# Performance work log

Hardware: AMD Instinct MI355X
Metric: run time of the kernel (lower is better)

Reference implementation:

```python
import jax, jax.numpy as jnp
import numpy as np

B, C, N = 16, 256, 2048
EPS = 1e-5


def setup_inputs() -> dict:
    key = jax.random.key(0)
    ks = jax.random.split(key, 8)
    s = 0.02
    return {
        "x": jax.random.normal(ks[0], (B, C, N), dtype=jnp.float32),
        "w_qkv": jax.random.normal(ks[1], (3 * C, C), dtype=jnp.float32) * s,
        "w_out": jax.random.normal(ks[2], (C, C), dtype=jnp.float32) * s,
        "b_out": jnp.zeros((C,), dtype=jnp.float32),
        "w_conv": jax.random.normal(ks[3], (C, C), dtype=jnp.float32) * s,
        "b_conv": jnp.zeros((C,), dtype=jnp.float32),
        "gamma": jnp.ones((C,), dtype=jnp.float32),
        "beta": jnp.zeros((C,), dtype=jnp.float32),
    }


def reference(x, w_qkv, w_out, b_out, w_conv, b_conv, gamma, beta):
    # x: [B, C, N]
    xt = jnp.swapaxes(x, 1, 2)                      # [B, N, C]
    qkv = jnp.einsum('bnc,dc->bnd', xt, w_qkv)      # [B, N, 3C]
    q, k, v = jnp.split(qkv, 3, axis=-1)
    scale = q.shape[-1] ** -0.5                     # single head, head_dim = C
    scores = jnp.einsum('bic,bjc->bij', q, k) * scale
    attn = jax.nn.softmax(scores, axis=-1)
    x_r = jnp.einsum('bij,bjc->bic', attn, v)
    x_r = jnp.einsum('bnc,oc->bno', x_r, w_out) + b_out  # output projection
    # offset attention: (x_t - x_r), back to [B, C, N]
    d = jnp.swapaxes(xt - x_r, 1, 2)
    # 1x1 conv
    y = jnp.einsum('oc,bcn->bon', w_conv, d) + b_conv[:, None]
    # BatchNorm1d (training-mode batch stats, biased variance)
    mean = jnp.mean(y, axis=(0, 2), keepdims=True)
    var = jnp.var(y, axis=(0, 2), keepdims=True)
    y = (y - mean) * jax.lax.rsqrt(var + EPS)
    y = y * gamma[:, None] + beta[:, None]
    return x + jax.nn.relu(y)
```

## Files before the change

kernel.cpp:

```cpp
#include <hip/hip_runtime.h>

#define BB 16
#define CC 256
#define NN 2048
#define QPRE 0.25f
#define KPRE 0.36067376f

typedef __attribute__((ext_vector_type(8))) short short8;
typedef __attribute__((ext_vector_type(8))) __bf16 bf16x8;
typedef __attribute__((ext_vector_type(4))) short s16x4;
typedef __attribute__((ext_vector_type(4))) float f32x4;
typedef __attribute__((ext_vector_type(16))) float f32x16;
typedef __attribute__((ext_vector_type(4))) int int4v;
typedef __attribute__((ext_vector_type(8))) int int8v;
typedef __attribute__((ext_vector_type(2))) long l64x2;

#define DEVI static __device__ __forceinline__

struct ABArg {
  short8 v;
  __device__ operator short8() const { return v; }
  __device__ operator bf16x8() const { return __builtin_bit_cast(bf16x8, v); }
};

DEVI f32x16 mfma32(short8 a, short8 b, f32x16 c) {
  return __builtin_amdgcn_mfma_f32_32x32x16_bf16(ABArg{a}, ABArg{b}, c, 0, 0, 0);
}
DEVI f32x16 mfma8(long a, long b, f32x16 c) {
  return __builtin_amdgcn_mfma_f32_32x32x16_fp8_fp8(a, b, c, 0, 0, 0);
}
DEVI f32x16 mfma8s(int8v a, int8v b, f32x16 c) {
  return __builtin_amdgcn_mfma_scale_f32_32x32x64_f8f6f4(a, b, c, 0, 0, 0, 127, 0, 127);
}

DEVI unsigned short f2bf(float f) {
  unsigned u = __builtin_bit_cast(unsigned, f);
  u = (u + 0x7fffu + ((u >> 16) & 1u)) >> 16;
  return (unsigned short)u;
}
DEVI float bf2f(unsigned short u) {
  unsigned x = (unsigned)u << 16;
  return __builtin_bit_cast(float, x);
}
DEVI unsigned char f2fp8(float f) {
  int r = __builtin_amdgcn_cvt_pk_fp8_f32(f, f, 0, false);
  return (unsigned char)(r & 0xff);
}
DEVI int psi(int c) { return (c & ~24) | ((c & 8) << 1) | ((c & 16) >> 1); }

DEVI void gl_lds16(const void* g, void* l) {
  __builtin_amdgcn_global_load_lds(
      (const __attribute__((address_space(1))) void*)g,
      (__attribute__((address_space(3))) void*)l, 16, 0, 0);
}

DEVI void stage64(const char* src, char* dst, int tid) {
#pragma unroll
  for (int i = 0; i < 8; i++) {
    int ch = tid + 256 * i;
    int row = ch >> 5, slot = ch & 31;
    gl_lds16(src + (size_t)row * 512 + ((slot * 16) ^ ((row & 7) << 4)), dst + ch * 16);
  }
}

DEVI short8 ldsfrag(const char* lds, int row, int kc, int h) {
  return *(const short8*)(lds + row * 512 + ((kc * 32 + h * 16) ^ ((row & 7) << 4)));
}

DEVI int drow(int r, int h) { return (r & 3) + 8 * (r >> 2) + 4 * h; }

DEVI int8v cat8(int4v lo, int4v hi) {
  int8v v;
  v[0] = lo[0]; v[1] = lo[1]; v[2] = lo[2]; v[3] = lo[3];
  v[4] = hi[0]; v[5] = hi[1]; v[6] = hi[2]; v[7] = hi[3];
  return v;
}

__global__ __launch_bounds__(256) void k_prep(const float* wq, const float* wc, const float* wo,
                                              const float* b_out, const float* b_conv,
                                              unsigned short* wq_b, unsigned short* wc_b,
                                              unsigned short* woT_b, float* biasv) {
  __shared__ float tile[64][65];
  int bx = blockIdx.x;
  if (bx < 768) {
    int i = bx * 256 + threadIdx.x;
    wq_b[i] = f2bf(wq[i]);
    if (i < CC * CC) wc_b[i] = f2bf(wc[i]);
  } else if (bx < 784) {
    int rb = bx - 768;
    int n0 = (rb & 3) * 64, c0 = (rb >> 2) * 64;
    int tcol = threadIdx.x & 63, trq = threadIdx.x >> 6;
#pragma unroll
    for (int rr = 0; rr < 16; rr++) {
      int cl = rr * 4 + trq;
      tile[cl][tcol] = wo[(size_t)(c0 + cl) * CC + n0 + tcol];
    }
    __syncthreads();
#pragma unroll
    for (int rr = 0; rr < 16; rr++) {
      int nl = rr * 4 + trq;
      woT_b[(size_t)(n0 + nl) * CC + c0 + tcol] = f2bf(tile[tcol][nl]);
    }
  } else {
    int o = (bx - 784) * 4 + (threadIdx.x >> 6);
    int lane = threadIdx.x & 63;
    f32x4 wv = *(const f32x4*)(wc + (size_t)o * CC + lane * 4);
    f32x4 bv = *(const f32x4*)(b_out + lane * 4);
    float s = wv[0] * bv[0] + wv[1] * bv[1] + wv[2] * bv[2] + wv[3] * bv[3];
#pragma unroll
    for (int d = 1; d < 64; d <<= 1) s += __shfl_xor(s, d, 64);
    if (lane == 0) biasv[o] = b_conv[o] - s;
  }
}

__global__ __launch_bounds__(256) void k_wcc(const unsigned short* wc_b,
                                             const unsigned short* woT_b, unsigned short* wccN) {
  __shared__ unsigned short WT[64 * 256];
  int o0 = blockIdx.x * 128, c0 = blockIdx.y * 64;
  int tid = threadIdx.x, lane = tid & 63, w = tid >> 6;
  int l31 = lane & 31, h = lane >> 5;
  stage64((const char*)(woT_b + (size_t)c0 * CC), (char*)WT, tid);
  int orow = o0 + w * 32 + l31;
  short8 aw[16];
  const unsigned short* Wp = wc_b + (size_t)orow * CC;
#pragma unroll
  for (int kc = 0; kc < 16; kc++) aw[kc] = *(const short8*)(Wp + kc * 16 + h * 8);
  __syncthreads();
  const char* Wl = (const char*)WT;
  f32x16 acc[2];
#pragma unroll
  for (int t = 0; t < 2; t++) {
#pragma unroll
    for (int r = 0; r < 16; r++) acc[t][r] = 0.f;
#pragma unroll
    for (int kc = 0; kc < 16; kc++)
      acc[t] = mfma32(aw[kc], ldsfrag(Wl, t * 32 + l31, kc, h), acc[t]);
  }
#pragma unroll
  for (int t = 0; t < 2; t++)
#pragma unroll
    for (int r = 0; r < 16; r++) {
      int od = o0 + w * 32 + drow(r, h);
      wccN[(size_t)od * CC + c0 + t * 32 + l31] = f2bf(-acc[t][r]);
    }
}

__global__ __launch_bounds__(256) void k_transpose(const float* x, unsigned short* xt) {
  __shared__ unsigned short tile[64][65];
  int b = blockIdx.z, c0 = blockIdx.y * 64, n0 = blockIdx.x * 64;
  int tcol = threadIdx.x & 63, trq = threadIdx.x >> 6;
  const float* xp = x + (size_t)b * CC * NN;
#pragma unroll
  for (int rr = 0; rr < 16; rr++) {
    int cl = rr * 4 + trq;
    tile[cl][tcol] = f2bf(xp[(size_t)(c0 + cl) * NN + n0 + tcol]);
  }
  __syncthreads();
  unsigned short* xtp = xt + (size_t)b * NN * CC;
#pragma unroll
  for (int rr = 0; rr < 16; rr++) {
    int nl = rr * 4 + trq;
    xtp[(size_t)(n0 + nl) * CC + c0 + tcol] = tile[tcol][nl];
  }
}

__global__ __launch_bounds__(256, 2) void k_qkv(const unsigned short* xt,
                                                const unsigned short* wqkv_b, unsigned char* Qf,
                                                unsigned char* Kf, unsigned char* Vf) {
  __shared__ unsigned short XT[2][64 * 256];
  int o0 = blockIdx.x * 128;
  int tok_base = blockIdx.y * 256;
  int tid = threadIdx.x, lane = tid & 63, w = tid >> 6;
  int l31 = lane & 31, h = lane >> 5;

  short8 aw[16];
  const unsigned short* Wp = wqkv_b + (size_t)(o0 + w * 32 + l31) * CC;
#pragma unroll
  for (int kc = 0; kc < 16; kc++) aw[kc] = *(const short8*)(Wp + kc * 16 + h * 8);

  const char* Xg = (const char*)xt;
  stage64(Xg + (size_t)tok_base * 512, (char*)XT[0], tid);
  __syncthreads();

  int od_l = o0 + w * 32 + l31;
  int psiod = psi(od_l & 255);
  int psil31 = psi(l31);

  int cur = 0;
  for (int tt = 0; tt < 4; tt++) {
    if (tt < 3)
      stage64(Xg + (size_t)(tok_base + (tt + 1) * 64) * 512, (char*)XT[cur ^ 1], tid);
    const char* Xl = (const char*)XT[cur];
    f32x16 acc[2];
#pragma unroll
    for (int t = 0; t < 2; t++)
#pragma unroll
      for (int r = 0; r < 16; r++) acc[t][r] = 0.f;
    if (o0 < 512) {
#pragma unroll
      for (int kc = 0; kc < 16; kc++) {
        acc[0] = mfma32(ldsfrag(Xl, l31, kc, h), aw[kc], acc[0]);
        acc[1] = mfma32(ldsfrag(Xl, 32 + l31, kc, h), aw[kc], acc[1]);
      }
    } else {
#pragma unroll
      for (int kc = 0; kc < 16; kc++) {
        acc[0] = mfma32(aw[kc], ldsfrag(Xl, l31, kc, h), acc[0]);
        acc[1] = mfma32(aw[kc], ldsfrag(Xl, 32 + l31, kc, h), acc[1]);
      }
    }
    int tok0 = tok_base + tt * 64;
    if (o0 < 256) {
#pragma unroll
      for (int t = 0; t < 2; t++)
#pragma unroll
        for (int r = 0; r < 16; r++) {
          int token = tok0 + t * 32 + drow(r, h);
          Qf[(size_t)token * 256 + psiod] = f2fp8(acc[t][r] * QPRE);
        }
    } else if (o0 < 512) {
#pragma unroll
      for (int t = 0; t < 2; t++)
#pragma unroll
        for (int r = 0; r < 16; r++) {
          int token = tok0 + t * 32 + drow(r, h);
          Kf[(size_t)token * 256 + psiod] = f2fp8(acc[t][r]);
        }
    } else {
      int bb = tok0 >> 11;
      int nnb = tok0 & 2047;
#pragma unroll
      for (int t = 0; t < 2; t++)
#pragma unroll
        for (int r = 0; r < 16; r++) {
          int od = o0 + w * 32 + drow(r, h) - 512;
          Vf[(size_t)bb * 256 * NN + (size_t)od * NN + nnb + t * 32 + psil31] = f2fp8(acc[t][r]);
        }
    }
    __syncthreads();
    cur ^= 1;
  }
}

__global__ __launch_bounds__(256, 2) void k_attn(const unsigned char* Qf, const unsigned char* Kf,
                                                 const unsigned char* Vf, unsigned short* AO) {
  __shared__ char SMEM[81920];
  int bid = blockIdx.x;
  int b = bid & 15;
  int q0 = (bid >> 4) * 64;
  int tid = threadIdx.x;
  int lane = tid & 63, w = tid >> 6;
  int g = w >> 1, p = w & 1;
  int gtid = tid & 127;
  int l31 = lane & 31, h = lane >> 5;

  char* G = SMEM + g * 40960;

  int qrow = q0 + p * 32 + l31;
  const unsigned char* Qp = Qf + (size_t)b * NN * 256 + (size_t)qrow * 256;
  int8v q32[4];
#pragma unroll
  for (int m = 0; m < 4; m++) {
    int4v lo = *(const int4v*)(Qp + m * 64 + h * 32);
    int4v hi = *(const int4v*)(Qp + m * 64 + h * 32 + 16);
    q32[m] = cat8(lo, hi);
  }

  f32x16 o[8];
#pragma unroll
  for (int i = 0; i < 8; i++)
#pragma unroll
    for (int r = 0; r < 16; r++) o[i][r] = 0.f;
  float lsum = 0.f;

  const unsigned char* Kg8 = Kf + (size_t)b * NN * 256;
  const unsigned char* Vg8 = Vf + (size_t)b * 256 * NN;
  int jbase = g * 1024;
  int swzk = (l31 & 7) << 4;

  auto stage_k = [&](char* dst, int j0) {
#pragma unroll
    for (int i = 0; i < 4; i++) {
      int ch = gtid + 128 * i;
      int row = ch >> 4, slot = ch & 15;
      gl_lds16(Kg8 + (size_t)(j0 + row) * 256 + ((slot * 16) ^ ((row & 7) << 4)), dst + ch * 16);
    }
  };
  auto stage_v = [&](char* dst, int j0) {
#pragma unroll
    for (int i = 0; i < 4; i++) {
      int ch = gtid + 128 * i;
      int row = ch >> 1, slot = ch & 1;
      gl_lds16(Vg8 + (size_t)row * 2048 + j0 + ((slot * 16) ^ (((row >> 2) & 1) << 4)),
               dst + ch * 16);
    }
  };

  stage_k(G, jbase);
  stage_v(G + 16384, jbase);
  __syncthreads();

  long pf0p = 0, pf1p = 0;
  for (int t = 0; t < 32; t++) {
    char* Kc = G + (t & 1) * 8192;
    if (t < 31) {
      int j0n = jbase + (t + 1) * 32;
      stage_k(G + ((t + 1) & 1) * 8192, j0n);
      stage_v(G + 16384 + ((t + 1) % 3) * 8192, j0n);
    }

    f32x16 s;
#pragma unroll
    for (int r = 0; r < 16; r++) s[r] = 0.f;
    __builtin_amdgcn_s_setprio(1);
#pragma unroll
    for (int m = 0; m < 4; m++) {
      int base = l31 * 256;
      int4v lo = *(const int4v*)(Kc + base + ((m * 64 + h * 32) ^ swzk));
      int4v hi = *(const int4v*)(Kc + base + ((m * 64 + h * 32 + 16) ^ swzk));
      s = mfma8s(cat8(lo, hi), q32[m], s);
    }
    __builtin_amdgcn_s_setprio(0);

    if (t > 0) {
      char* Vp = G + 16384 + ((t - 1) % 3) * 8192;
      int swzv = ((l31 >> 2) & 1) << 4;
      __builtin_amdgcn_s_setprio(1);
#pragma unroll
      for (int ct = 0; ct < 8; ct++) {
        l64x2 vv = *(const l64x2*)(Vp + (ct * 32 + l31) * 32 + ((h * 16) ^ swzv));
        o[ct] = mfma8(pf0p, vv[0], o[ct]);
        o[ct] = mfma8(pf1p, vv[1], o[ct]);
      }
      __builtin_amdgcn_s_setprio(0);
    }

    float pv[16];
    float rsum = 0.f;
#pragma unroll
    for (int r = 0; r < 16; r++) {
      pv[r] = __builtin_amdgcn_exp2f(s[r]);
      rsum += pv[r];
    }
    lsum += rsum;

    int P0 = __builtin_amdgcn_cvt_pk_fp8_f32(pv[0], pv[1], 0, false);
    P0 = __builtin_amdgcn_cvt_pk_fp8_f32(pv[2], pv[3], P0, true);
    int P1 = __builtin_amdgcn_cvt_pk_fp8_f32(pv[4], pv[5], 0, false);
    P1 = __builtin_amdgcn_cvt_pk_fp8_f32(pv[6], pv[7], P1, true);
    int P2 = __builtin_amdgcn_cvt_pk_fp8_f32(pv[8], pv[9], 0, false);
    P2 = __builtin_amdgcn_cvt_pk_fp8_f32(pv[10], pv[11], P2, true);
    int P3 = __builtin_amdgcn_cvt_pk_fp8_f32(pv[12], pv[13], 0, false);
    P3 = __builtin_amdgcn_cvt_pk_fp8_f32(pv[14], pv[15], P3, true);
    int x0 = P0, y0 = P1;
    asm volatile("v_permlane32_swap_b32 %0, %1" : "+v"(x0), "+v"(y0));
    int x1 = P2, y1 = P3;
    asm volatile("v_permlane32_swap_b32 %0, %1" : "+v"(x1), "+v"(y1));
    long pf0c = ((long)(unsigned)y0 << 32) | (unsigned)x0;
    long pf1c = ((long)(unsigned)y1 << 32) | (unsigned)x1;

    __syncthreads();
    pf0p = pf0c;
    pf1p = pf1c;
  }

  {
    char* Vp = G + 16384 + (31 % 3) * 8192;
    int swzv = ((l31 >> 2) & 1) << 4;
#pragma unroll
    for (int ct = 0; ct < 8; ct++) {
      l64x2 vv = *(const l64x2*)(Vp + (ct * 32 + l31) * 32 + ((h * 16) ^ swzv));
      o[ct] = mfma8(pf0p, vv[0], o[ct]);
      o[ct] = mfma8(pf1p, vv[1], o[ct]);
    }
  }

  lsum += __shfl_xor(lsum, 32, 64);
  float* Lx = (float*)SMEM;
  if (h == 0) Lx[w * 32 + l31] = lsum;
  __syncthreads();
  float ltot = lsum + Lx[(w ^ 2) * 32 + l31];
  float linv[16];
#pragma unroll
  for (int r = 0; r < 16; r++) linv[r] = 1.f / __shfl(ltot, drow(r, h), 64);
  __syncthreads();

  char* Rb = SMEM + p * 32768;
  if (g == 1) {
#pragma unroll
    for (int ct = 0; ct < 8; ct++)
#pragma unroll
      for (int k = 0; k < 4; k++) {
        f32x4 v = {o[ct][4 * k], o[ct][4 * k + 1], o[ct][4 * k + 2], o[ct][4 * k + 3]};
        *(f32x4*)(Rb + ((ct * 4 + k) * 64 + lane) * 16) = v;
      }
  }
  __syncthreads();
  if (g == 0) {
    unsigned short* AOp = AO + (size_t)b * NN * CC;
#pragma unroll
    for (int ct = 0; ct < 8; ct++)
#pragma unroll
      for (int k = 0; k < 4; k++) {
        f32x4 qv = *(const f32x4*)(Rb + ((ct * 4 + k) * 64 + lane) * 16);
#pragma unroll
        for (int j = 0; j < 4; j++) {
          int r = 4 * k + j;
          float v = (o[ct][r] + qv[j]) * linv[r];
          AOp[(size_t)(q0 + p * 32 + drow(r, h)) * CC + ct * 32 + l31] = f2bf(v);
        }
      }
  }
}

__global__ __launch_bounds__(256, 1) void k_fused(const unsigned short* xt,
                                                  const unsigned short* AO,
                                                  const unsigned short* wc_b,
                                                  const unsigned short* wccN, const float* biasv,
                                                  unsigned short* yT, float* psum, float* psq) {
  __shared__ unsigned short XT[2][64 * 256], AL[2][64 * 256];
  int o0 = blockIdx.x * 128;
  int tok_base = blockIdx.y * 256;
  int tid = threadIdx.x, lane = tid & 63, w = tid >> 6;
  int l31 = lane & 31, h = lane >> 5;
  int od = o0 + w * 32 + l31;

  short8 aw[32];
  const unsigned short* Wp1 = wc_b + (size_t)od * CC;
  const unsigned short* Wp2 = wccN + (size_t)od * CC;
#pragma unroll
  for (int kc = 0; kc < 16; kc++) {
    aw[kc] = *(const short8*)(Wp1 + kc * 16 + h * 8);
    aw[16 + kc] = *(const short8*)(Wp2 + kc * 16 + h * 8);
  }
  float bias_l = biasv[od];
  float sacc = 0.f, qacc = 0.f;

  const char* Xg = (const char*)xt;
  const char* Ag = (const char*)AO;
  stage64(Xg + (size_t)tok_base * 512, (char*)XT[0], tid);
  stage64(Ag + (size_t)tok_base * 512, (char*)AL[0], tid);
  __syncthreads();

  int cur = 0;
  for (int tt = 0; tt < 4; tt++) {
    if (tt < 3) {
      stage64(Xg + (size_t)(tok_base + (tt + 1) * 64) * 512, (char*)XT[cur ^ 1], tid);
      stage64(Ag + (size_t)(tok_base + (tt + 1) * 64) * 512, (char*)AL[cur ^ 1], tid);
    }
    const char* Xl = (const char*)XT[cur];
    const char* Al = (const char*)AL[cur];
    f32x16 acc[2];
#pragma unroll
    for (int t = 0; t < 2; t++)
#pragma unroll
      for (int r = 0; r < 16; r++) acc[t][r] = 0.f;
#pragma unroll
    for (int kc = 0; kc < 16; kc++) {
      acc[0] = mfma32(ldsfrag(Xl, l31, kc, h), aw[kc], acc[0]);
      acc[1] = mfma32(ldsfrag(Xl, 32 + l31, kc, h), aw[kc], acc[1]);
    }
#pragma unroll
    for (int kc = 0; kc < 16; kc++) {
      acc[0] = mfma32(ldsfrag(Al, l31, kc, h), aw[16 + kc], acc[0]);
      acc[1] = mfma32(ldsfrag(Al, 32 + l31, kc, h), aw[16 + kc], acc[1]);
    }
    int tok0 = tok_base + tt * 64;
#pragma unroll
    for (int t = 0; t < 2; t++)
#pragma unroll
      for (int r = 0; r < 16; r++) {
        float v = acc[t][r] + bias_l;
        sacc += v;
        qacc += v * v;
        int token = tok0 + t * 32 + drow(r, h);
        yT[(size_t)token * CC + od] = f2bf(v);
      }
    __syncthreads();
    cur ^= 1;
  }

  sacc += __shfl_xor(sacc, 32, 64);
  qacc += __shfl_xor(qacc, 32, 64);
  if (h == 0) {
    psum[blockIdx.y * 256 + od] = sacc;
    psq[blockIdx.y * 256 + od] = qacc;
  }
}

__global__ __launch_bounds__(1024) void k_stats2(const float* psum, const float* psq,
                                                 const float* gamma, const float* beta,
                                                 float* scale, float* shift) {
  __shared__ float S4[4][256], Q4[4][256];
  int o = threadIdx.x & 255, part = threadIdx.x >> 8;
  float S = 0.f, Q = 0.f;
  for (int b = part * 32; b < part * 32 + 32; b++) {
    S += psum[b * 256 + o];
    Q += psq[b * 256 + o];
  }
  S4[part][o] = S;
  Q4[part][o] = Q;
  __syncthreads();
  if (part == 0) {
    S = S4[0][o] + S4[1][o] + S4[2][o] + S4[3][o];
    Q = Q4[0][o] + Q4[1][o] + Q4[2][o] + Q4[3][o];
    const float inv = 1.f / (BB * NN);
    float mean = S * inv;
    float var = Q * inv - mean * mean;
    float rstd = rsqrtf(var + 1e-5f);
    float sc = gamma[o] * rstd;
    scale[o] = sc;
    shift[o] = beta[o] - mean * sc;
  }
}

__global__ __launch_bounds__(256) void k_final(const unsigned short* yT, const float* x,
                                               const float* scale, const float* shift, float* out) {
  __shared__ float tile[64][65];
  int n0 = blockIdx.x * 64, c0 = blockIdx.y * 64, b = blockIdx.z;
  int tid = threadIdx.x;
#pragma unroll
  for (int it = 0; it < 2; it++) {
    int rowl = (tid >> 3) + it * 32, slot = tid & 7;
    short8 v = *(const short8*)(yT + (size_t)(b * NN + n0 + rowl) * CC + c0 + slot * 8);
#pragma unroll
    for (int j = 0; j < 8; j++) tile[rowl][slot * 8 + j] = bf2f((unsigned short)v[j]);
  }
  __syncthreads();
  int nl = tid & 63, cg = tid >> 6;
  size_t xb = (size_t)b * CC * NN;
#pragma unroll
  for (int i = 0; i < 16; i++) {
    int cl = cg * 16 + i;
    int c = c0 + cl;
    float v = tile[nl][cl] * scale[c] + shift[c];
    size_t idx = xb + (size_t)c * NN + n0 + nl;
    out[idx] = x[idx] + fmaxf(v, 0.f);
  }
}

extern "C" void kernel_launch(void* const* d_in, const int* in_sizes, int n_in,
                              void* d_out, int out_size, void* d_ws, size_t ws_size,
                              hipStream_t stream) {
  const float* x      = (const float*)d_in[0];
  const float* w_qkv  = (const float*)d_in[1];
  const float* w_out  = (const float*)d_in[2];
  const float* b_out  = (const float*)d_in[3];
  const float* w_conv = (const float*)d_in[4];
  const float* b_conv = (const float*)d_in[5];
  const float* gamma  = (const float*)d_in[6];
  const float* beta   = (const float*)d_in[7];
  float* out = (float*)d_out;

  char* ws = (char*)d_ws;
  size_t off = 0;
  auto take = [&](size_t bytes) -> char* {
    char* p = ws + off;
    off += (bytes + 255) & ~(size_t)255;
    return p;
  };
  const size_t BNC  = (size_t)BB * NN * CC;
  unsigned char* Qf  = (unsigned char*)take(BNC);
  unsigned char* Kf  = (unsigned char*)take(BNC);
  unsigned char* Vf  = (unsigned char*)take(BNC);
  unsigned short* xt = (unsigned short*)take(BNC * 2);
  unsigned short* AO = (unsigned short*)take(BNC * 2);
  unsigned short* wq_b = (unsigned short*)take((size_t)3 * CC * CC * 2);
  unsigned short* wc_b = (unsigned short*)take((size_t)CC * CC * 2);
  unsigned short* woT_b= (unsigned short*)take((size_t)CC * CC * 2);
  unsigned short* wccN = (unsigned short*)take((size_t)CC * CC * 2);
  float* biasv = (float*)take(CC * 4);
  float* psum  = (float*)take(128 * CC * 4);
  float* psq   = (float*)take(128 * CC * 4);
  float* scale = (float*)take(CC * 4);
  float* shift = (float*)take(CC * 4);
  unsigned short* yT = (unsigned short*)Qf;

  k_prep<<<848, 256, 0, stream>>>(w_qkv, w_conv, w_out, b_out, b_conv, wq_b, wc_b, woT_b, biasv);
  k_wcc<<<dim3(2, 4), 256, 0, stream>>>(wc_b, woT_b, wccN);
  k_transpose<<<dim3(32, 4, BB), 256, 0, stream>>>(x, xt);
  k_qkv<<<dim3(6, 128), 256, 0, stream>>>(xt, wq_b, Qf, Kf, Vf);
  k_attn<<<512, 256, 0, stream>>>(Qf, Kf, Vf, AO);
  k_fused<<<dim3(2, 128), 256, 0, stream>>>(xt, AO, wc_b, wccN, biasv, yT, psum, psq);
  k_stats2<<<1, 1024, 0, stream>>>(psum, psq, gamma, beta, scale, shift);
  k_final<<<dim3(32, 4, BB), 256, 0, stream>>>(yT, x, scale, shift, out);
}
```

Before: 148.9 us.

## Batch two key tiles per PV step using K=64 scaled fp8 MFMA

Instead of issuing two K=16 fp8 MFMAs per output tile on every iteration (one iteration late), the P fragments from two consecutive 32-key tiles are collected and one 32x32x64 scaled fp8 MFMA per output tile is issued on odd iterations. Each lane half reads V from a different buffer of the triple-buffered ring. This cuts the MFMA instruction count and the V-read overhead, and drops the one-iteration software pipelining of PV behind QK. In exchange, QK and PV work are no longer interleaved across iterations, and the V triple buffer must still hold the previous tile when it is consumed.

```diff
diff --git a/kernel.cpp b/kernel.cpp
--- a/kernel.cpp
+++ b/kernel.cpp
@@ -277,6 +277,7 @@
   const unsigned char* Vg8 = Vf + (size_t)b * 256 * NN;
   int jbase = g * 1024;
   int swzk = (l31 & 7) << 4;
+  int swzv = ((l31 >> 2) & 1) << 4;
 
   auto stage_k = [&](char* dst, int j0) {
 #pragma unroll
@@ -300,7 +301,7 @@
   stage_v(G + 16384, jbase);
   __syncthreads();
 
-  long pf0p = 0, pf1p = 0;
+  int ps0 = 0, ps1 = 0, ps2 = 0, ps3 = 0;
   for (int t = 0; t < 32; t++) {
     char* Kc = G + (t & 1) * 8192;
     if (t < 31) {
@@ -322,19 +323,6 @@
     }
     __builtin_amdgcn_s_setprio(0);
 
-    if (t > 0) {
-      char* Vp = G + 16384 + ((t - 1) % 3) * 8192;
-      int swzv = ((l31 >> 2) & 1) << 4;
-      __builtin_amdgcn_s_setprio(1);
-#pragma unroll
-      for (int ct = 0; ct < 8; ct++) {
-        l64x2 vv = *(const l64x2*)(Vp + (ct * 32 + l31) * 32 + ((h * 16) ^ swzv));
-        o[ct] = mfma8(pf0p, vv[0], o[ct]);
-        o[ct] = mfma8(pf1p, vv[1], o[ct]);
-      }
-      __builtin_amdgcn_s_setprio(0);
-    }
-
     float pv[16];
     float rsum = 0.f;
 #pragma unroll
@@ -344,35 +332,44 @@
     }
     lsum += rsum;
 
-    int P0 = __builtin_amdgcn_cvt_pk_fp8_f32(pv[0], pv[1], 0, false);
-    P0 = __builtin_amdgcn_cvt_pk_fp8_f32(pv[2], pv[3], P0, true);
-    int P1 = __builtin_amdgcn_cvt_pk_fp8_f32(pv[4], pv[5], 0, false);
-    P1 = __builtin_amdgcn_cvt_pk_fp8_f32(pv[6], pv[7], P1, true);
-    int P2 = __builtin_amdgcn_cvt_pk_fp8_f32(pv[8], pv[9], 0, false);
-    P2 = __builtin_amdgcn_cvt_pk_fp8_f32(pv[10], pv[11], P2, true);
-    int P3 = __builtin_amdgcn_cvt_pk_fp8_f32(pv[12], pv[13], 0, false);
-    P3 = __builtin_amdgcn_cvt_pk_fp8_f32(pv[14], pv[15], P3, true);
-    int x0 = P0, y0 = P1;
-    asm volatile("v_permlane32_swap_b32 %0, %1" : "+v"(x0), "+v"(y0));
-    int x1 = P2, y1 = P3;
-    asm volatile("v_permlane32_swap_b32 %0, %1" : "+v"(x1), "+v"(y1));
-    long pf0c = ((long)(unsigned)y0 << 32) | (unsigned)x0;
-    long pf1c = ((long)(unsigned)y1 << 32) | (unsigned)x1;
+    int C0 = __builtin_amdgcn_cvt_pk_fp8_f32(pv[0], pv[1], 0, false);
+    C0 = __builtin_amdgcn_cvt_pk_fp8_f32(pv[2], pv[3], C0, true);
+    int C1 = __builtin_amdgcn_cvt_pk_fp8_f32(pv[4], pv[5], 0, false);
+    C1 = __builtin_amdgcn_cvt_pk_fp8_f32(pv[6], pv[7], C1, true);
+    int C2 = __builtin_amdgcn_cvt_pk_fp8_f32(pv[8], pv[9], 0, false);
+    C2 = __builtin_amdgcn_cvt_pk_fp8_f32(pv[10], pv[11], C2, true);
+    int C3 = __builtin_amdgcn_cvt_pk_fp8_f32(pv[12], pv[13], 0, false);
+    C3 = __builtin_amdgcn_cvt_pk_fp8_f32(pv[14], pv[15], C3, true);
+
+    if ((t & 1) == 0) {
+      ps0 = C0; ps1 = C1; ps2 = C2; ps3 = C3;
+    } else {
+      int x0 = ps0, y0 = C0;
+      asm volatile("v_permlane32_swap_b32 %0, %1" : "+v"(x0), "+v"(y0));
+      int x1 = ps1, y1 = C1;
+      asm volatile("v_permlane32_swap_b32 %0, %1" : "+v"(x1), "+v"(y1));
+      int x2 = ps2, y2 = C2;
+      asm volatile("v_permlane32_swap_b32 %0, %1" : "+v"(x2), "+v"(y2));
+      int x3 = ps3, y3 = C3;
+      asm volatile("v_permlane32_swap_b32 %0, %1" : "+v"(x3), "+v"(y3));
+      int8v pa;
+      pa[0] = x0; pa[1] = y0;
+      pa[2] = x2; pa[3] = y2;
+      pa[4] = x1; pa[5] = y1;
+      pa[6] = x3; pa[7] = y3;
+      char* Vh = G + 16384 + ((t - 1 + h) % 3) * 8192;
+      __builtin_amdgcn_s_setprio(1);
+#pragma unroll
+      for (int ct = 0; ct < 8; ct++) {
+        int rowb = (ct * 32 + l31) * 32;
+        int4v lo = *(const int4v*)(Vh + rowb + (0 ^ swzv));
+        int4v hi = *(const int4v*)(Vh + rowb + (16 ^ swzv));
+        o[ct] = mfma8s(pa, cat8(lo, hi), o[ct]);
+      }
+      __builtin_amdgcn_s_setprio(0);
+    }
 
     __syncthreads();
-    pf0p = pf0c;
-    pf1p = pf1c;
-  }
-
-  {
-    char* Vp = G + 16384 + (31 % 3) * 8192;
-    int swzv = ((l31 >> 2) & 1) << 4;
-#pragma unroll
-    for (int ct = 0; ct < 8; ct++) {
-      l64x2 vv = *(const l64x2*)(Vp + (ct * 32 + l31) * 32 + ((h * 16) ^ swzv));
-      o[ct] = mfma8(pf0p, vv[0], o[ct]);
-      o[ct] = mfma8(pf1p, vv[1], o[ct]);
-    }
   }
 
   lsum += __shfl_xor(lsum, 32, 64);
```

New measurement: 145.2 us. 1.03x faster.
